# Performance work log

Measured on AMD Instinct MI355X. Metric: run time of the kernel, lower is better.

Reference implementation:

```python
import jax, jax.numpy as jnp
import numpy as np

N = 100000      # nodes
R = 8           # relations
E_DIM = 128     # embedding dim
N_EDGES = 1600000  # n * avg_degree(16)


def setup_inputs() -> dict:
    key = jax.random.key(0)
    k1, k2, k3, k4, k5 = jax.random.split(key, 5)
    x = jax.random.normal(k1, (N, E_DIM), dtype=jnp.float32)
    # xavier-ish scale for (r, e, e) relation weights
    weights = jax.random.normal(k2, (R, E_DIM, E_DIM), dtype=jnp.float32) * (1.0 / np.sqrt(E_DIM))
    edge_rel = jax.random.randint(k3, (N_EDGES,), 0, R, dtype=jnp.int32)
    edge_src = jax.random.randint(k4, (N_EDGES,), 0, N, dtype=jnp.int32)
    edge_dst = jax.random.randint(k5, (N_EDGES,), 0, N, dtype=jnp.int32)
    return dict(x=x, weights=weights, edge_rel=edge_rel, edge_src=edge_src, edge_dst=edge_dst)


def reference(x, weights, edge_rel, edge_src, edge_dst):
    n, e = x.shape
    r = weights.shape[0]
    # sparse adjacency row index: relation-block row = rel * n + dst  (shape rn)
    rows = edge_rel.astype(jnp.int32) * n + edge_dst.astype(jnp.int32)
    # row-normalized values: vals = 1 / row_degree (util.sum_sparse)
    deg = jax.ops.segment_sum(jnp.ones(rows.shape, dtype=x.dtype), rows, num_segments=r * n)
    vals = 1.0 / deg[rows]  # only evaluated at rows with >=1 edge
    # SpMM: h = graph @ x, viewed as (r, n, e)
    msgs = vals[:, None] * x[edge_src]                       # (E, e) gather
    h = jax.ops.segment_sum(msgs, rows, num_segments=r * n)  # (r*n, e) scatter-add
    h = h.reshape(r, n, e)
    # per-relation transform: (r, e_out, e_in) x (r, n, e_in) -> (n, r, e_out)
    h = jnp.einsum('rih,rnh->nri', weights, h)
    # SumUnify: relu(sum over relations)
    return jax.nn.relu(h.sum(axis=1))
```

## Files before the change

### kernel.cpp

```cpp
#include <hip/hip_runtime.h>
#include <hip/hip_bf16.h>

#define ED 128
#define RR 8
#define KTOT (RR * ED)
#define LDB 136
#define CH 50048
#define HB 1568
#define CB 1600
#define WB 8

typedef __attribute__((ext_vector_type(8))) short short8;
typedef __attribute__((ext_vector_type(4))) float f32x4;
typedef __attribute__((ext_vector_type(4))) unsigned short u16x4;

#define RL(v, i) __builtin_amdgcn_readlane(v, i)

__device__ __forceinline__ unsigned short f2bf(float f){
  unsigned int u = __builtin_bit_cast(unsigned int, f);
  return (unsigned short)((u + 0x7fffu + ((u >> 16) & 1u)) >> 16);
}
__device__ __forceinline__ float bf2f(unsigned int lo){
  return __builtin_bit_cast(float, lo << 16);
}
__device__ __forceinline__ unsigned int packbf(float hi, float lo){
  return ((unsigned int)f2bf(hi) << 16) | f2bf(lo);
}
__device__ __forceinline__ void cast4(const float* __restrict__ in,
                                      unsigned short* __restrict__ out, int i){
  f32x4 v = __builtin_nontemporal_load((const f32x4*)(in + (size_t)i * 4));
  u16x4 o;
  o[0] = f2bf(v[0]); o[1] = f2bf(v[1]); o[2] = f2bf(v[2]); o[3] = f2bf(v[3]);
  *(u16x4*)(out + (size_t)i * 4) = o;
}

__global__ void fused_front(const int* __restrict__ rel, const int* __restrict__ dst,
                            unsigned int* __restrict__ rowcnt, int* __restrict__ rank,
                            const float* __restrict__ x, unsigned short* __restrict__ xb, int nx4,
                            const float* __restrict__ w, unsigned short* __restrict__ wb, int nw4,
                            int E){
  int b = blockIdx.x;
  if (b < HB){
    int tid = b * 256 + threadIdx.x;
    int nthr = HB * 256;
    int E4 = E >> 2;
    for (int i = tid; i < E4; i += nthr){
      int4 r4 = ((const int4*)rel)[i];
      int4 d4 = ((const int4*)dst)[i];
      int k0 = (d4.x << 3) | r4.x;
      int k1 = (d4.y << 3) | r4.y;
      int k2 = (d4.z << 3) | r4.z;
      int k3 = (d4.w << 3) | r4.w;
      unsigned o0 = atomicAdd(&rowcnt[k0 >> 1], (k0 & 1) ? 0x10000u : 1u);
      unsigned o1 = atomicAdd(&rowcnt[k1 >> 1], (k1 & 1) ? 0x10000u : 1u);
      unsigned o2 = atomicAdd(&rowcnt[k2 >> 1], (k2 & 1) ? 0x10000u : 1u);
      unsigned o3 = atomicAdd(&rowcnt[k3 >> 1], (k3 & 1) ? 0x10000u : 1u);
      int4 rk;
      rk.x = (k0 & 1) ? (int)(o0 >> 16) : (int)(o0 & 0xffffu);
      rk.y = (k1 & 1) ? (int)(o1 >> 16) : (int)(o1 & 0xffffu);
      rk.z = (k2 & 1) ? (int)(o2 >> 16) : (int)(o2 & 0xffffu);
      rk.w = (k3 & 1) ? (int)(o3 >> 16) : (int)(o3 & 0xffffu);
      ((int4*)rank)[i] = rk;
    }
  } else if (b < HB + CB){
    int tid = (b - HB) * 256 + threadIdx.x;
    int nthr = CB * 256;
    for (int i = tid; i < nx4; i += nthr) cast4(x, xb, i);
  } else {
    int tid = (b - HB - CB) * 256 + threadIdx.x;
    int nthr = WB * 256;
    for (int i = tid; i < nw4; i += nthr) cast4(w, wb, i);
  }
}

__launch_bounds__(1024)
__global__ void scan_block_sum(const unsigned int* __restrict__ rowcnt, int* __restrict__ bsum, int mm){
  __shared__ int lds[16];
  int t = threadIdx.x;
  int idx = blockIdx.x * 1024 + t;
  unsigned pv = (idx < mm) ? rowcnt[idx] : 0u;
  int v = (int)(pv & 0xffffu) + (int)(pv >> 16);
#pragma unroll
  for (int o = 32; o > 0; o >>= 1) v += __shfl_down(v, o);
  if ((t & 63) == 0) lds[t >> 6] = v;
  __syncthreads();
  if (t == 0){
    int s = 0;
#pragma unroll
    for (int w = 0; w < 16; ++w) s += lds[w];
    bsum[blockIdx.x] = s;
  }
}

__launch_bounds__(1024)
__global__ void scan_bsum_par(const int* __restrict__ bsum, int* __restrict__ bscan,
                              int nb, int* __restrict__ total_out){
  __shared__ int wsum[16];
  int t = threadIdx.x, lane = t & 63, wid = t >> 6;
  int v = (t < nb) ? bsum[t] : 0;
  int incl = v;
#pragma unroll
  for (int o = 1; o < 64; o <<= 1){
    int u = __shfl_up(incl, o);
    if (lane >= o) incl += u;
  }
  if (lane == 63) wsum[wid] = incl;
  __syncthreads();
  int woff = 0;
  for (int w0 = 0; w0 < wid; ++w0) woff += wsum[w0];
  if (t < nb) bscan[t] = woff + incl - v;
  if (t == nb - 1) *total_out = woff + incl;
}

__launch_bounds__(1024)
__global__ void scan_final(const unsigned int* __restrict__ rowcnt, const int* __restrict__ bscan,
                           int* __restrict__ row_ptr, int mm){
  __shared__ int wsum[16];
  int t = threadIdx.x, lane = t & 63, wid = t >> 6;
  int idx = blockIdx.x * 1024 + t;
  unsigned pv = (idx < mm) ? rowcnt[idx] : 0u;
  int lo = (int)(pv & 0xffffu);
  int v = lo + (int)(pv >> 16);
  int incl = v;
#pragma unroll
  for (int o = 1; o < 64; o <<= 1){
    int u = __shfl_up(incl, o);
    if (lane >= o) incl += u;
  }
  if (lane == 63) wsum[wid] = incl;
  __syncthreads();
  int woff = bscan[blockIdx.x];
  for (int w0 = 0; w0 < wid; ++w0) woff += wsum[w0];
  if (idx < mm){
    int ex = woff + incl - v;
    row_ptr[2 * idx]     = ex;
    row_ptr[2 * idx + 1] = ex + lo;
  }
}

__global__ void scatter_pos(const int* __restrict__ rel, const int* __restrict__ src,
                            const int* __restrict__ dst, const int* __restrict__ rank,
                            const int* __restrict__ row_ptr, int* __restrict__ payload, int E){
  int tid = blockIdx.x * 256 + threadIdx.x;
  int nthr = gridDim.x * 256;
  int E4 = E >> 2;
  for (int i = tid; i < E4; i += nthr){
    int4 r4 = ((const int4*)rel)[i];
    int4 s4 = ((const int4*)src)[i];
    int4 d4 = ((const int4*)dst)[i];
    int4 k4 = ((const int4*)rank)[i];
    int p0 = row_ptr[(d4.x << 3) | r4.x] + k4.x;
    int p1 = row_ptr[(d4.y << 3) | r4.y] + k4.y;
    int p2 = row_ptr[(d4.z << 3) | r4.z] + k4.z;
    int p3 = row_ptr[(d4.w << 3) | r4.w] + k4.w;
    payload[p0] = s4.x;
    payload[p1] = s4.y;
    payload[p2] = s4.z;
    payload[p3] = s4.w;
  }
}

__launch_bounds__(256)
__global__ void row_agg(const unsigned short* __restrict__ xb,
                        const int* __restrict__ row_ptr8,
                        const int* __restrict__ payload,
                        unsigned short* __restrict__ h2buf, int d0, int d1){
  int d    = d0 + ((blockIdx.x * 256 + threadIdx.x) >> 6);
  int lane = threadIdx.x & 63;
  if (d >= d1) return;

  int p9 = 0;
  if (lane < 9) p9 = row_ptr8[(d << 3) + lane];
  int b0  = RL(p9, 0);
  int o1  = RL(p9, 1) - b0;
  int o2  = RL(p9, 2) - b0;
  int o3  = RL(p9, 3) - b0;
  int o4  = RL(p9, 4) - b0;
  int o5  = RL(p9, 5) - b0;
  int o6  = RL(p9, 6) - b0;
  int o7  = RL(p9, 7) - b0;
  int cnt = RL(p9, 8) - b0;

  float ax0=0.f,ay0=0.f,ax1=0.f,ay1=0.f,ax2=0.f,ay2=0.f,ax3=0.f,ay3=0.f;
  float ax4=0.f,ay4=0.f,ax5=0.f,ay5=0.f,ax6=0.f,ay6=0.f,ax7=0.f,ay7=0.f;

#define ROUTE(VV, IDX) { \
    float lo = bf2f((VV) & 0xffffu), hi = bf2f((VV) >> 16); \
    if ((IDX) < o4){ \
      if ((IDX) < o2){ if ((IDX) < o1){ ax0+=lo; ay0+=hi; } else { ax1+=lo; ay1+=hi; } } \
      else           { if ((IDX) < o3){ ax2+=lo; ay2+=hi; } else { ax3+=lo; ay3+=hi; } } \
    } else { \
      if ((IDX) < o6){ if ((IDX) < o5){ ax4+=lo; ay4+=hi; } else { ax5+=lo; ay5+=hi; } } \
      else           { if ((IDX) < o7){ ax6+=lo; ay6+=hi; } else { ax7+=lo; ay7+=hi; } } \
    } }

  if (cnt <= 64){
    int pl = payload[b0 + lane];
    int e = 0;
    for (; e + 8 <= cnt; e += 8){
      int s0 = RL(pl, e);
      int s1 = RL(pl, e + 1);
      int s2 = RL(pl, e + 2);
      int s3 = RL(pl, e + 3);
      int s4 = RL(pl, e + 4);
      int s5 = RL(pl, e + 5);
      int s6 = RL(pl, e + 6);
      int s7 = RL(pl, e + 7);
      unsigned int v0 = ((const unsigned int*)(xb + ((size_t)s0 << 7)))[lane];
      unsigned int v1 = ((const unsigned int*)(xb + ((size_t)s1 << 7)))[lane];
      unsigned int v2 = ((const unsigned int*)(xb + ((size_t)s2 << 7)))[lane];
      unsigned int v3 = ((const unsigned int*)(xb + ((size_t)s3 << 7)))[lane];
      unsigned int v4 = ((const unsigned int*)(xb + ((size_t)s4 << 7)))[lane];
      unsigned int v5 = ((const unsigned int*)(xb + ((size_t)s5 << 7)))[lane];
      unsigned int v6 = ((const unsigned int*)(xb + ((size_t)s6 << 7)))[lane];
      unsigned int v7 = ((const unsigned int*)(xb + ((size_t)s7 << 7)))[lane];
      ROUTE(v0, e)
      ROUTE(v1, e + 1)
      ROUTE(v2, e + 2)
      ROUTE(v3, e + 3)
      ROUTE(v4, e + 4)
      ROUTE(v5, e + 5)
      ROUTE(v6, e + 6)
      ROUTE(v7, e + 7)
    }
    for (; e < cnt; ++e){
      int s = RL(pl, e);
      unsigned int v = ((const unsigned int*)(xb + ((size_t)s << 7)))[lane];
      ROUTE(v, e)
    }
  } else {
    for (int e = 0; e < cnt; ++e){
      int s = __builtin_amdgcn_readfirstlane(payload[b0 + e]);
      unsigned int v = ((const unsigned int*)(xb + ((size_t)s << 7)))[lane];
      ROUTE(v, e)
    }
  }
#undef ROUTE

  int c0 = o1, c1 = o2 - o1, c2 = o3 - o2, c3 = o4 - o3;
  int c4 = o5 - o4, c5 = o6 - o5, c6 = o7 - o6, c7 = cnt - o7;
  unsigned int* hp = (unsigned int*)h2buf + ((size_t)(d - d0) << 9) + lane;
  float sc;
  sc = c0 ? 1.f / (float)c0 : 0.f; hp[0]   = packbf(ay0*sc, ax0*sc);
  sc = c1 ? 1.f / (float)c1 : 0.f; hp[64]  = packbf(ay1*sc, ax1*sc);
  sc = c2 ? 1.f / (float)c2 : 0.f; hp[128] = packbf(ay2*sc, ax2*sc);
  sc = c3 ? 1.f / (float)c3 : 0.f; hp[192] = packbf(ay3*sc, ax3*sc);
  sc = c4 ? 1.f / (float)c4 : 0.f; hp[256] = packbf(ay4*sc, ax4*sc);
  sc = c5 ? 1.f / (float)c5 : 0.f; hp[320] = packbf(ay5*sc, ax5*sc);
  sc = c6 ? 1.f / (float)c6 : 0.f; hp[384] = packbf(ay6*sc, ax6*sc);
  sc = c7 ? 1.f / (float)c7 : 0.f; hp[448] = packbf(ay7*sc, ax7*sc);
}

__launch_bounds__(256)
__global__ void gemm_out(const unsigned short* __restrict__ h2buf,
                         const unsigned short* __restrict__ wbb,
                         float* __restrict__ out, int d0, int d1){
  __shared__ __align__(16) unsigned short lds_a[128 * LDB];
  __shared__ __align__(16) unsigned short lds_b[128 * LDB];
  const int t = threadIdx.x;
  const int wave = t >> 6, lane = t & 63;
  const int wr = wave >> 1, wc = wave & 1;
  const int dbase = d0 + blockIdx.x * 128;
  const int frow = lane & 15, kb = lane >> 4;

  f32x4 acc[4][4];
#pragma unroll
  for (int rt = 0; rt < 4; ++rt)
#pragma unroll
    for (int jt = 0; jt < 4; ++jt)
      acc[rt][jt] = (f32x4){0.f, 0.f, 0.f, 0.f};

  short8 pa[8], pb[8];
#pragma unroll
  for (int p = 0; p < 8; ++p){
    int q = p * 256 + t;
    int row = q >> 4, col = q & 15;
    int gr = dbase + row; if (gr >= d1) gr = d1 - 1;
    pa[p] = *(const short8*)(h2buf + (size_t)(gr - d0) * KTOT + col * 8);
    pb[p] = *(const short8*)(wbb + row * ED + col * 8);
  }

  for (int r = 0; r < RR; ++r){
    __syncthreads();
#pragma unroll
    for (int p = 0; p < 8; ++p){
      int q = p * 256 + t;
      int row = q >> 4, col = q & 15;
      *(short8*)&lds_a[row * LDB + col * 8] = pa[p];
      *(short8*)&lds_b[row * LDB + col * 8] = pb[p];
    }
    __syncthreads();

    if (r + 1 < RR){
#pragma unroll
      for (int p = 0; p < 8; ++p){
        int q = p * 256 + t;
        int row = q >> 4, col = q & 15;
        int gr = dbase + row; if (gr >= d1) gr = d1 - 1;
        pa[p] = *(const short8*)(h2buf + (size_t)(gr - d0) * KTOT + (r + 1) * ED + col * 8);
        pb[p] = *(const short8*)(wbb + (size_t)(r + 1) * ED * ED + row * ED + col * 8);
      }
    }

    short8 a[4][4], b[4][4];
#pragma unroll
    for (int rt = 0; rt < 4; ++rt)
#pragma unroll
      for (int ks = 0; ks < 4; ++ks)
        a[rt][ks] = *(const short8*)&lds_a[(wr * 64 + rt * 16 + frow) * LDB + ks * 32 + kb * 8];
#pragma unroll
    for (int jt = 0; jt < 4; ++jt)
#pragma unroll
      for (int ks = 0; ks < 4; ++ks)
        b[jt][ks] = *(const short8*)&lds_b[(wc * 64 + jt * 16 + frow) * LDB + ks * 32 + kb * 8];
#pragma unroll
    for (int rt = 0; rt < 4; ++rt)
#pragma unroll
      for (int jt = 0; jt < 4; ++jt)
#pragma unroll
        for (int ks = 0; ks < 4; ++ks)
          acc[rt][jt] = __builtin_amdgcn_mfma_f32_16x16x32_bf16(a[rt][ks], b[jt][ks], acc[rt][jt], 0, 0, 0);
  }

  const int drow = (lane >> 4) * 4;
  const int dcol = lane & 15;
#pragma unroll
  for (int rt = 0; rt < 4; ++rt)
#pragma unroll
    for (int jt = 0; jt < 4; ++jt)
#pragma unroll
      for (int reg = 0; reg < 4; ++reg){
        int i = dbase + wr * 64 + rt * 16 + drow + reg;
        if (i < d1)
          __builtin_nontemporal_store(fmaxf(acc[rt][jt][reg], 0.f),
                                      &out[(size_t)i * ED + wc * 64 + jt * 16 + dcol]);
      }
}

extern "C" void kernel_launch(void* const* d_in, const int* in_sizes, int n_in,
                              void* d_out, int out_size, void* d_ws, size_t ws_size,
                              hipStream_t stream){
  const float* x  = (const float*)d_in[0];
  const float* w  = (const float*)d_in[1];
  const int* erel = (const int*)d_in[2];
  const int* esrc = (const int*)d_in[3];
  const int* edst = (const int*)d_in[4];
  float* out = (float*)d_out;

  const int n = in_sizes[0] / ED;
  const int E = in_sizes[2];
  const int m = n * RR;
  const int mm = m / 2;
  const int NB = (mm + 1023) / 1024;

  char* ws = (char*)d_ws;
  size_t off = 0;
  auto alloc = [&](size_t bytes) -> char* {
    char* p = ws + off;
    off += (bytes + 255) & ~(size_t)255;
    return p;
  };
  unsigned short* h2buf   = (unsigned short*)alloc((size_t)CH * KTOT * 2);
  unsigned short* xb      = (unsigned short*)alloc((size_t)n * ED * 2);
  unsigned short* wbb     = (unsigned short*)alloc((size_t)RR * ED * ED * 2);
  int*            payload = (int*)alloc((size_t)E * 4);
  int*            row_ptr = (int*)alloc((size_t)(m + 1) * 4);
  unsigned int*   rowcnt  = (unsigned int*)alloc((size_t)mm * 4);
  int*            rank    = (int*)alloc((size_t)E * 4);
  int*            bsum    = (int*)alloc((size_t)NB * 4);
  int*            bscan   = (int*)alloc((size_t)NB * 4);
  if (off > ws_size || NB > 1024) return;

  (void)hipMemsetAsync(rowcnt, 0, (size_t)mm * 4, stream);

  fused_front  <<<HB + CB + WB, 256, 0, stream>>>(erel, edst, rowcnt, rank,
                                                  x, xb, n * ED / 4,
                                                  w, wbb, RR * ED * ED / 4, E);
  scan_block_sum<<<NB, 1024, 0, stream>>>(rowcnt, bsum, mm);
  scan_bsum_par<<<1, 1024, 0, stream>>>(bsum, bscan, NB, row_ptr + m);
  scan_final   <<<NB, 1024, 0, stream>>>(rowcnt, bscan, row_ptr, mm);
  scatter_pos  <<<1568, 256, 0, stream>>>(erel, esrc, edst, rank, row_ptr, payload, E);

  for (int c = 0; c < 2; ++c){
    int d0 = c * CH;
    int d1 = (c == 0) ? CH : n;
    int nodes = d1 - d0;
    row_agg <<<(nodes + 3) / 4, 256, 0, stream>>>(xb, row_ptr, payload, h2buf, d0, d1);
    gemm_out<<<(nodes + 127) / 128, 256, 0, stream>>>(h2buf, wbb, out, d0, d1);
  }
}
```

Before: 283.8 us.

## Transform node features per relation before aggregation and fuse GEMM into front kernel

Reorders the computation so each node's features are first multiplied by all eight relation weights (Z = x·W_r, stored as bf16 n×1024) inside the front kernel, interleaved with the histogram blocks. The aggregation kernel then gathers the relation-specific transformed rows per edge, normalises, sums across relations, applies ReLU and writes the output directly. This removes the separate h2buf intermediate, the chunked row_agg/gemm_out launches and the standalone bf16 casts. In exchange the gather reads from a much larger Z buffer (8x the size of xb), so per-edge gathers have less cache locality, and an extra bf16 rounding sits on the transformed values.

```diff
diff --git a/kernel.cpp b/kernel.cpp
--- a/kernel.cpp
+++ b/kernel.cpp
@@ -5,13 +5,11 @@
 #define RR 8
 #define KTOT (RR * ED)
 #define LDB 136
-#define CH 50048
-#define HB 1568
-#define CB 1600
-#define WB 8
+#define HB 768
 
 typedef __attribute__((ext_vector_type(8))) short short8;
 typedef __attribute__((ext_vector_type(4))) float f32x4;
+typedef __attribute__((ext_vector_type(2))) float f32x2;
 typedef __attribute__((ext_vector_type(4))) unsigned short u16x4;
 
 #define RL(v, i) __builtin_amdgcn_readlane(v, i)
@@ -23,25 +21,22 @@
 __device__ __forceinline__ float bf2f(unsigned int lo){
   return __builtin_bit_cast(float, lo << 16);
 }
-__device__ __forceinline__ unsigned int packbf(float hi, float lo){
-  return ((unsigned int)f2bf(hi) << 16) | f2bf(lo);
-}
-__device__ __forceinline__ void cast4(const float* __restrict__ in,
-                                      unsigned short* __restrict__ out, int i){
-  f32x4 v = __builtin_nontemporal_load((const f32x4*)(in + (size_t)i * 4));
-  u16x4 o;
-  o[0] = f2bf(v[0]); o[1] = f2bf(v[1]); o[2] = f2bf(v[2]); o[3] = f2bf(v[3]);
-  *(u16x4*)(out + (size_t)i * 4) = o;
-}
 
 __global__ void fused_front(const int* __restrict__ rel, const int* __restrict__ dst,
-                            unsigned int* __restrict__ rowcnt, int* __restrict__ rank,
-                            const float* __restrict__ x, unsigned short* __restrict__ xb, int nx4,
-                            const float* __restrict__ w, unsigned short* __restrict__ wb, int nw4,
-                            int E){
+                            unsigned int* __restrict__ rowcnt, int* __restrict__ rank, int E,
+                            const float* __restrict__ x, const float* __restrict__ w,
+                            unsigned short* __restrict__ z, int n, int nzb){
+  __shared__ __align__(16) unsigned short lds_a[128 * LDB];
+  __shared__ __align__(16) unsigned short lds_b[128 * LDB];
+
   int b = blockIdx.x;
-  if (b < HB){
-    int tid = b * 256 + threadIdx.x;
+  int npair = HB < nzb ? HB : nzb;
+  bool isZ; int id;
+  if (b < 2 * npair){ isZ = !(b & 1); id = b >> 1; }
+  else { id = npair + (b - 2 * npair); isZ = (nzb > npair); }
+
+  if (!isZ){
+    int tid = id * 256 + threadIdx.x;
     int nthr = HB * 256;
     int E4 = E >> 2;
     for (int i = tid; i < E4; i += nthr){
@@ -62,14 +57,76 @@
       rk.w = (k3 & 1) ? (int)(o3 >> 16) : (int)(o3 & 0xffffu);
       ((int4*)rank)[i] = rk;
     }
-  } else if (b < HB + CB){
-    int tid = (b - HB) * 256 + threadIdx.x;
-    int nthr = CB * 256;
-    for (int i = tid; i < nx4; i += nthr) cast4(x, xb, i);
-  } else {
-    int tid = (b - HB - CB) * 256 + threadIdx.x;
-    int nthr = WB * 256;
-    for (int i = tid; i < nw4; i += nthr) cast4(w, wb, i);
+    return;
+  }
+
+  const int t = threadIdx.x;
+  const int wave = t >> 6, lane = t & 63;
+  const int wr = wave >> 1, wc = wave & 1;
+  const int dbase = id * 128;
+  const int frow = lane & 15, kb = lane >> 4;
+
+#pragma unroll
+  for (int p = 0; p < 16; ++p){
+    int q = p * 256 + t;
+    int row = q >> 5, c4 = q & 31;
+    int gr = dbase + row; if (gr >= n) gr = n - 1;
+    f32x4 v = __builtin_nontemporal_load((const f32x4*)(x + (size_t)gr * ED + c4 * 4));
+    u16x4 o; o[0] = f2bf(v[0]); o[1] = f2bf(v[1]); o[2] = f2bf(v[2]); o[3] = f2bf(v[3]);
+    *(u16x4*)&lds_a[row * LDB + c4 * 4] = o;
+  }
+
+  for (int nt = 0; nt < RR; ++nt){
+    __syncthreads();
+    const float* wp = w + (size_t)nt * ED * ED;
+#pragma unroll
+    for (int p = 0; p < 16; ++p){
+      int q = p * 256 + t;
+      int row = q >> 5, c4 = q & 31;
+      f32x4 v = *(const f32x4*)(wp + (size_t)row * ED + c4 * 4);
+      u16x4 o; o[0] = f2bf(v[0]); o[1] = f2bf(v[1]); o[2] = f2bf(v[2]); o[3] = f2bf(v[3]);
+      *(u16x4*)&lds_b[row * LDB + c4 * 4] = o;
+    }
+    __syncthreads();
+
+    f32x4 acc[4][4];
+#pragma unroll
+    for (int rt = 0; rt < 4; ++rt)
+#pragma unroll
+      for (int jt = 0; jt < 4; ++jt)
+        acc[rt][jt] = (f32x4){0.f, 0.f, 0.f, 0.f};
+
+    short8 a[4][4], bf[4][4];
+#pragma unroll
+    for (int rt = 0; rt < 4; ++rt)
+#pragma unroll
+      for (int ks = 0; ks < 4; ++ks)
+        a[rt][ks] = *(const short8*)&lds_a[(wr * 64 + rt * 16 + frow) * LDB + ks * 32 + kb * 8];
+#pragma unroll
+    for (int jt = 0; jt < 4; ++jt)
+#pragma unroll
+      for (int ks = 0; ks < 4; ++ks)
+        bf[jt][ks] = *(const short8*)&lds_b[(wc * 64 + jt * 16 + frow) * LDB + ks * 32 + kb * 8];
+#pragma unroll
+    for (int rt = 0; rt < 4; ++rt)
+#pragma unroll
+      for (int jt = 0; jt < 4; ++jt)
+#pragma unroll
+        for (int ks = 0; ks < 4; ++ks)
+          acc[rt][jt] = __builtin_amdgcn_mfma_f32_16x16x32_bf16(a[rt][ks], bf[jt][ks], acc[rt][jt], 0, 0, 0);
+
+    const int drow = (lane >> 4) * 4;
+    const int dcol = lane & 15;
+#pragma unroll
+    for (int rt = 0; rt < 4; ++rt)
+#pragma unroll
+      for (int jt = 0; jt < 4; ++jt)
+#pragma unroll
+        for (int reg = 0; reg < 4; ++reg){
+          int i = dbase + wr * 64 + rt * 16 + drow + reg;
+          if (i < n)
+            z[(size_t)i * KTOT + nt * ED + wc * 64 + jt * 16 + dcol] = f2bf(acc[rt][jt][reg]);
+        }
   }
 }
 
@@ -149,25 +206,21 @@
     int4 s4 = ((const int4*)src)[i];
     int4 d4 = ((const int4*)dst)[i];
     int4 k4 = ((const int4*)rank)[i];
-    int p0 = row_ptr[(d4.x << 3) | r4.x] + k4.x;
-    int p1 = row_ptr[(d4.y << 3) | r4.y] + k4.y;
-    int p2 = row_ptr[(d4.z << 3) | r4.z] + k4.z;
-    int p3 = row_ptr[(d4.w << 3) | r4.w] + k4.w;
-    payload[p0] = s4.x;
-    payload[p1] = s4.y;
-    payload[p2] = s4.z;
-    payload[p3] = s4.w;
+    payload[row_ptr[(d4.x << 3) | r4.x] + k4.x] = s4.x;
+    payload[row_ptr[(d4.y << 3) | r4.y] + k4.y] = s4.y;
+    payload[row_ptr[(d4.z << 3) | r4.z] + k4.z] = s4.z;
+    payload[row_ptr[(d4.w << 3) | r4.w] + k4.w] = s4.w;
   }
 }
 
 __launch_bounds__(256)
-__global__ void row_agg(const unsigned short* __restrict__ xb,
+__global__ void agg_out(const unsigned short* __restrict__ z,
                         const int* __restrict__ row_ptr8,
                         const int* __restrict__ payload,
-                        unsigned short* __restrict__ h2buf, int d0, int d1){
-  int d    = d0 + ((blockIdx.x * 256 + threadIdx.x) >> 6);
+                        float* __restrict__ out, int n){
+  int d    = (blockIdx.x * 256 + threadIdx.x) >> 6;
   int lane = threadIdx.x & 63;
-  if (d >= d1) return;
+  if (d >= n) return;
 
   int p9 = 0;
   if (lane < 9) p9 = row_ptr8[(d << 3) + lane];
@@ -184,6 +237,9 @@
   float ax0=0.f,ay0=0.f,ax1=0.f,ay1=0.f,ax2=0.f,ay2=0.f,ax3=0.f,ay3=0.f;
   float ax4=0.f,ay4=0.f,ax5=0.f,ay5=0.f,ax6=0.f,ay6=0.f,ax7=0.f,ay7=0.f;
 
+#define RSEL(IDX) (((IDX) >= o1) + ((IDX) >= o2) + ((IDX) >= o3) + ((IDX) >= o4) + \
+                   ((IDX) >= o5) + ((IDX) >= o6) + ((IDX) >= o7))
+#define ZROW(S, IDX) ((const unsigned int*)(z + ((size_t)(((S) << 3) | RSEL(IDX)) << 7)))[lane]
 #define ROUTE(VV, IDX) { \
     float lo = bf2f((VV) & 0xffffu), hi = bf2f((VV) >> 16); \
     if ((IDX) < o4){ \
@@ -206,14 +262,14 @@
       int s5 = RL(pl, e + 5);
       int s6 = RL(pl, e + 6);
       int s7 = RL(pl, e + 7);
-      unsigned int v0 = ((const unsigned int*)(xb + ((size_t)s0 << 7)))[lane];
-      unsigned int v1 = ((const unsigned int*)(xb + ((size_t)s1 << 7)))[lane];
-      unsigned int v2 = ((const unsigned int*)(xb + ((size_t)s2 << 7)))[lane];
-      unsigned int v3 = ((const unsigned int*)(xb + ((size_t)s3 << 7)))[lane];
-      unsigned int v4 = ((const unsigned int*)(xb + ((size_t)s4 << 7)))[lane];
-      unsigned int v5 = ((const unsigned int*)(xb + ((size_t)s5 << 7)))[lane];
-      unsigned int v6 = ((const unsigned int*)(xb + ((size_t)s6 << 7)))[lane];
-      unsigned int v7 = ((const unsigned int*)(xb + ((size_t)s7 << 7)))[lane];
+      unsigned int v0 = ZROW(s0, e);
+      unsigned int v1 = ZROW(s1, e + 1);
+      unsigned int v2 = ZROW(s2, e + 2);
+      unsigned int v3 = ZROW(s3, e + 3);
+      unsigned int v4 = ZROW(s4, e + 4);
+      unsigned int v5 = ZROW(s5, e + 5);
+      unsigned int v6 = ZROW(s6, e + 6);
+      unsigned int v7 = ZROW(s7, e + 7);
       ROUTE(v0, e)
       ROUTE(v1, e + 1)
       ROUTE(v2, e + 2)
@@ -225,116 +281,34 @@
     }
     for (; e < cnt; ++e){
       int s = RL(pl, e);
-      unsigned int v = ((const unsigned int*)(xb + ((size_t)s << 7)))[lane];
+      unsigned int v = ZROW(s, e);
       ROUTE(v, e)
     }
   } else {
     for (int e = 0; e < cnt; ++e){
       int s = __builtin_amdgcn_readfirstlane(payload[b0 + e]);
-      unsigned int v = ((const unsigned int*)(xb + ((size_t)s << 7)))[lane];
+      unsigned int v = ZROW(s, e);
       ROUTE(v, e)
     }
   }
 #undef ROUTE
+#undef ZROW
+#undef RSEL
 
   int c0 = o1, c1 = o2 - o1, c2 = o3 - o2, c3 = o4 - o3;
   int c4 = o5 - o4, c5 = o6 - o5, c6 = o7 - o6, c7 = cnt - o7;
-  unsigned int* hp = (unsigned int*)h2buf + ((size_t)(d - d0) << 9) + lane;
-  float sc;
-  sc = c0 ? 1.f / (float)c0 : 0.f; hp[0]   = packbf(ay0*sc, ax0*sc);
-  sc = c1 ? 1.f / (float)c1 : 0.f; hp[64]  = packbf(ay1*sc, ax1*sc);
-  sc = c2 ? 1.f / (float)c2 : 0.f; hp[128] = packbf(ay2*sc, ax2*sc);
-  sc = c3 ? 1.f / (float)c3 : 0.f; hp[192] = packbf(ay3*sc, ax3*sc);
-  sc = c4 ? 1.f / (float)c4 : 0.f; hp[256] = packbf(ay4*sc, ax4*sc);
-  sc = c5 ? 1.f / (float)c5 : 0.f; hp[320] = packbf(ay5*sc, ax5*sc);
-  sc = c6 ? 1.f / (float)c6 : 0.f; hp[384] = packbf(ay6*sc, ax6*sc);
-  sc = c7 ? 1.f / (float)c7 : 0.f; hp[448] = packbf(ay7*sc, ax7*sc);
-}
-
-__launch_bounds__(256)
-__global__ void gemm_out(const unsigned short* __restrict__ h2buf,
-                         const unsigned short* __restrict__ wbb,
-                         float* __restrict__ out, int d0, int d1){
-  __shared__ __align__(16) unsigned short lds_a[128 * LDB];
-  __shared__ __align__(16) unsigned short lds_b[128 * LDB];
-  const int t = threadIdx.x;
-  const int wave = t >> 6, lane = t & 63;
-  const int wr = wave >> 1, wc = wave & 1;
-  const int dbase = d0 + blockIdx.x * 128;
-  const int frow = lane & 15, kb = lane >> 4;
-
-  f32x4 acc[4][4];
-#pragma unroll
-  for (int rt = 0; rt < 4; ++rt)
-#pragma unroll
-    for (int jt = 0; jt < 4; ++jt)
-      acc[rt][jt] = (f32x4){0.f, 0.f, 0.f, 0.f};
-
-  short8 pa[8], pb[8];
-#pragma unroll
-  for (int p = 0; p < 8; ++p){
-    int q = p * 256 + t;
-    int row = q >> 4, col = q & 15;
-    int gr = dbase + row; if (gr >= d1) gr = d1 - 1;
-    pa[p] = *(const short8*)(h2buf + (size_t)(gr - d0) * KTOT + col * 8);
-    pb[p] = *(const short8*)(wbb + row * ED + col * 8);
-  }
-
-  for (int r = 0; r < RR; ++r){
-    __syncthreads();
-#pragma unroll
-    for (int p = 0; p < 8; ++p){
-      int q = p * 256 + t;
-      int row = q >> 4, col = q & 15;
-      *(short8*)&lds_a[row * LDB + col * 8] = pa[p];
-      *(short8*)&lds_b[row * LDB + col * 8] = pb[p];
-    }
-    __syncthreads();
-
-    if (r + 1 < RR){
-#pragma unroll
-      for (int p = 0; p < 8; ++p){
-        int q = p * 256 + t;
-        int row = q >> 4, col = q & 15;
-        int gr = dbase + row; if (gr >= d1) gr = d1 - 1;
-        pa[p] = *(const short8*)(h2buf + (size_t)(gr - d0) * KTOT + (r + 1) * ED + col * 8);
-        pb[p] = *(const short8*)(wbb + (size_t)(r + 1) * ED * ED + row * ED + col * 8);
-      }
-    }
-
-    short8 a[4][4], b[4][4];
-#pragma unroll
-    for (int rt = 0; rt < 4; ++rt)
-#pragma unroll
-      for (int ks = 0; ks < 4; ++ks)
-        a[rt][ks] = *(const short8*)&lds_a[(wr * 64 + rt * 16 + frow) * LDB + ks * 32 + kb * 8];
-#pragma unroll
-    for (int jt = 0; jt < 4; ++jt)
-#pragma unroll
-      for (int ks = 0; ks < 4; ++ks)
-        b[jt][ks] = *(const short8*)&lds_b[(wc * 64 + jt * 16 + frow) * LDB + ks * 32 + kb * 8];
-#pragma unroll
-    for (int rt = 0; rt < 4; ++rt)
-#pragma unroll
-      for (int jt = 0; jt < 4; ++jt)
-#pragma unroll
-        for (int ks = 0; ks < 4; ++ks)
-          acc[rt][jt] = __builtin_amdgcn_mfma_f32_16x16x32_bf16(a[rt][ks], b[jt][ks], acc[rt][jt], 0, 0, 0);
-  }
-
-  const int drow = (lane >> 4) * 4;
-  const int dcol = lane & 15;
-#pragma unroll
-  for (int rt = 0; rt < 4; ++rt)
-#pragma unroll
-    for (int jt = 0; jt < 4; ++jt)
-#pragma unroll
-      for (int reg = 0; reg < 4; ++reg){
-        int i = dbase + wr * 64 + rt * 16 + drow + reg;
-        if (i < d1)
-          __builtin_nontemporal_store(fmaxf(acc[rt][jt][reg], 0.f),
-                                      &out[(size_t)i * ED + wc * 64 + jt * 16 + dcol]);
-      }
+  float ox = 0.f, oy = 0.f, sc;
+  sc = c0 ? 1.f / (float)c0 : 0.f; ox += ax0 * sc; oy += ay0 * sc;
+  sc = c1 ? 1.f / (float)c1 : 0.f; ox += ax1 * sc; oy += ay1 * sc;
+  sc = c2 ? 1.f / (float)c2 : 0.f; ox += ax2 * sc; oy += ay2 * sc;
+  sc = c3 ? 1.f / (float)c3 : 0.f; ox += ax3 * sc; oy += ay3 * sc;
+  sc = c4 ? 1.f / (float)c4 : 0.f; ox += ax4 * sc; oy += ay4 * sc;
+  sc = c5 ? 1.f / (float)c5 : 0.f; ox += ax5 * sc; oy += ay5 * sc;
+  sc = c6 ? 1.f / (float)c6 : 0.f; ox += ax6 * sc; oy += ay6 * sc;
+  sc = c7 ? 1.f / (float)c7 : 0.f; ox += ax7 * sc; oy += ay7 * sc;
+
+  f32x2 ov = { fmaxf(ox, 0.f), fmaxf(oy, 0.f) };
+  __builtin_nontemporal_store(ov, (f32x2*)(out + (size_t)d * ED) + lane);
 }
 
 extern "C" void kernel_launch(void* const* d_in, const int* in_sizes, int n_in,
@@ -352,6 +326,7 @@
   const int m = n * RR;
   const int mm = m / 2;
   const int NB = (mm + 1023) / 1024;
+  const int NZB = (n + 127) / 128;
 
   char* ws = (char*)d_ws;
   size_t off = 0;
@@ -360,32 +335,24 @@
     off += (bytes + 255) & ~(size_t)255;
     return p;
   };
-  unsigned short* h2buf   = (unsigned short*)alloc((size_t)CH * KTOT * 2);
-  unsigned short* xb      = (unsigned short*)alloc((size_t)n * ED * 2);
-  unsigned short* wbb     = (unsigned short*)alloc((size_t)RR * ED * ED * 2);
+  unsigned short* z       = (unsigned short*)alloc((size_t)n * KTOT * 2);
   int*            payload = (int*)alloc((size_t)E * 4);
   int*            row_ptr = (int*)alloc((size_t)(m + 1) * 4);
+  int*            rank    = (int*)alloc((size_t)E * 4);
   unsigned int*   rowcnt  = (unsigned int*)alloc((size_t)mm * 4);
-  int*            rank    = (int*)alloc((size_t)E * 4);
   int*            bsum    = (int*)alloc((size_t)NB * 4);
   int*            bscan   = (int*)alloc((size_t)NB * 4);
   if (off > ws_size || NB > 1024) return;
 
   (void)hipMemsetAsync(rowcnt, 0, (size_t)mm * 4, stream);
 
-  fused_front  <<<HB + CB + WB, 256, 0, stream>>>(erel, edst, rowcnt, rank,
-                                                  x, xb, n * ED / 4,
-                                                  w, wbb, RR * ED * ED / 4, E);
+  int npair = HB < NZB ? HB : NZB;
+  int grid_front = (HB - npair) + (NZB - npair) + 2 * npair;
+  fused_front  <<<grid_front, 256, 0, stream>>>(erel, edst, rowcnt, rank, E,
+                                                x, w, z, n, NZB);
   scan_block_sum<<<NB, 1024, 0, stream>>>(rowcnt, bsum, mm);
   scan_bsum_par<<<1, 1024, 0, stream>>>(bsum, bscan, NB, row_ptr + m);
   scan_final   <<<NB, 1024, 0, stream>>>(rowcnt, bscan, row_ptr, mm);
   scatter_pos  <<<1568, 256, 0, stream>>>(erel, esrc, edst, rank, row_ptr, payload, E);
-
-  for (int c = 0; c < 2; ++c){
-    int d0 = c * CH;
-    int d1 = (c == 0) ? CH : n;
-    int nodes = d1 - d0;
-    row_agg <<<(nodes + 3) / 4, 256, 0, stream>>>(xb, row_ptr, payload, h2buf, d0, d1);
-    gemm_out<<<(nodes + 127) / 128, 256, 0, stream>>>(h2buf, wbb, out, d0, d1);
-  }
-}
+  agg_out      <<<(n + 3) / 4, 256, 0, stream>>>(z, row_ptr, payload, out, n);
+}
```

After: 437.4 us. +54.1%, slower.
